# Performance work log

Measured on AMD Instinct MI355X. Metric: run time of the kernel, lower is better.

## Reference

```python
import jax, jax.numpy as jnp
import numpy as np
import math

DIM = 1024
SEQ = 4096
BATCH = 4
CHUNK = 64
LN_EPS = 1e-5


def setup_inputs() -> dict:
    key = jax.random.key(0)
    ks = jax.random.split(key, 16)
    d = DIM
    def lin(k):
        k1, k2 = jax.random.split(k)
        lim = 1.0 / math.sqrt(d)
        W = jax.random.uniform(k1, (d, d), jnp.float32, -lim, lim)
        b = jax.random.uniform(k2, (d,), jnp.float32, -lim, lim)
        return W, b
    Wk, bk = lin(ks[0])
    Wv, bv = lin(ks[1])
    Wq, bq = lin(ks[2])
    Wkm, bkm = lin(ks[3])
    Wqm, bqm = lin(ks[4])
    Wo, bo = lin(ks[5])
    return {
        "x": jax.random.normal(ks[6], (BATCH, SEQ, d), jnp.float32),
        "base_phases": jax.random.normal(ks[7], (SEQ, d), jnp.float32) * math.pi,
        "Wk": Wk, "bk": bk, "Wv": Wv, "bv": bv, "Wq": Wq, "bq": bq,
        "Wkm": Wkm, "bkm": bkm, "Wqm": Wqm, "bqm": bqm,
        "mod_scale": jnp.ones((1,), jnp.float32) * 0.1,
        "ln_g": jnp.ones((d,), jnp.float32),
        "ln_b": jnp.zeros((d,), jnp.float32),
        "Wo": Wo, "bo": bo,
    }


def reference(x, base_phases, Wk, bk, Wv, bv, Wq, bq, Wkm, bkm, Wqm, bqm,
              mod_scale, ln_g, ln_b, Wo, bo):
    B, S, D = x.shape
    key = x @ Wk + bk
    value = x @ Wv + bv
    query = x @ Wq + bq
    base = base_phases[:S][None]                      # [1,S,D]
    key_phase = base + (key @ Wkm + bkm) * mod_scale   # [B,S,D]
    query_phase = base + (query @ Wqm + bqm) * mod_scale
    bound_real = value * jnp.cos(key_phase)
    bound_imag = value * jnp.sin(key_phase)
    pad = (CHUNK - S % CHUNK) % CHUNK
    if pad > 0:
        pcfg = ((0, 0), (0, pad), (0, 0))
        bound_real = jnp.pad(bound_real, pcfg)
        bound_imag = jnp.pad(bound_imag, pcfg)
        query_phase = jnp.pad(query_phase, pcfg)
    P = S + pad
    nc = P // CHUNK
    br = bound_real.reshape(B, nc, CHUNK, D)
    bi = bound_imag.reshape(B, nc, CHUNK, D)
    qp = query_phase.reshape(B, nc, CHUNK, D)
    mem_real = jnp.cumsum(br, axis=2)
    mem_imag = jnp.cumsum(bi, axis=2)
    retrieved = mem_real * jnp.cos(qp) + mem_imag * jnp.sin(qp)
    retrieved = retrieved.reshape(B, P, D)[:, :S] / math.sqrt(D)
    mu = jnp.mean(retrieved, axis=-1, keepdims=True)
    var = jnp.mean(jnp.square(retrieved - mu), axis=-1, keepdims=True)
    normed = (retrieved - mu) * jax.lax.rsqrt(var + LN_EPS) * ln_g + ln_b
    out = normed @ Wo + bo
    return x + out
```

## Files before the change

### kernel.cpp

```cpp
#include <hip/hip_runtime.h>

#define DIM 1024
#define SEQ 4096
#define MROWS 16384
#define CHUNK 64
#define NCHUNKBLKS 256

typedef float  f32x4  __attribute__((ext_vector_type(4)));
typedef __bf16 bf16x8 __attribute__((ext_vector_type(8)));
typedef __bf16 bf16x4 __attribute__((ext_vector_type(4)));

__device__ __forceinline__ void gld16(const void* g, void* l) {
  __builtin_amdgcn_global_load_lds((__attribute__((address_space(1))) void*)g,
                                   (__attribute__((address_space(3))) void*)l,
                                   16, 0, 0);
}

__device__ __forceinline__ f32x4 ld4f(const __bf16* p) {
  bf16x4 v = *(const bf16x4*)p;
  f32x4 r;
#pragma unroll
  for (int j = 0; j < 4; ++j) r[j] = (float)v[j];
  return r;
}

template <int MODE, int NCOLT>
__global__ __launch_bounds__(512, 2)
void gemm256(const __bf16* __restrict__ A, const __bf16* __restrict__ Bt,
             const float* __restrict__ bias,
             __bf16* __restrict__ ob0, __bf16* __restrict__ ob1,
             __bf16* __restrict__ ob2,
             float* __restrict__ of, const float* __restrict__ xres)
{
  __shared__ __bf16 As[2][256 * 64];
  __shared__ __bf16 Bs[2][256 * 64];
  const int tid  = threadIdx.x;
  const int lane = tid & 63;
  const int widx = tid >> 6;
  const int wr = widx >> 2, wc = widx & 3;
  const int bx  = blockIdx.x;
  const int xcd = bx & 7, p = bx >> 3;
  const int row_t = (xcd << 3) + (p & 7);
  const int col_t = p >> 3;
  const int row0 = row_t * 256, col0 = col_t * 256;

  const int srow   = widx * 8 + (lane >> 3);
  const int schunk = (lane & 7) ^ ((lane >> 3) & 7);
  const __bf16* Ag = A  + (size_t)(row0 + srow) * DIM + schunk * 8;
  const __bf16* Bg = Bt + (size_t)(col0 + srow) * DIM + schunk * 8;

  f32x4 acc[8][4] = {};
  const int arb = wr * 128 + (lane & 15);
  const int brb = wc * 64  + (lane & 15);
  const int kg = lane >> 4;
  const int lx = lane & 7;

#define STG(kt_, bu_) { \
    const __bf16* a_ = Ag + (kt_) * 64; \
    const __bf16* b_ = Bg + (kt_) * 64; \
    char* ab_ = (char*)(&As[bu_][0]) + widx * 1024; \
    char* bb_ = (char*)(&Bs[bu_][0]) + widx * 1024; \
    _Pragma("unroll") for (int i_ = 0; i_ < 4; ++i_) { \
      gld16(a_ + i_ * 64 * DIM, ab_ + i_ * 8192); \
      gld16(b_ + i_ * 64 * DIM, bb_ + i_ * 8192); } }

  STG(0, 0)
  __syncthreads();
  for (int kt = 0; kt < 16; ++kt) {
    if (kt + 1 < 16) STG(kt + 1, (kt + 1) & 1)
    __builtin_amdgcn_sched_barrier(0);
    const bf16x8* Av = (const bf16x8*)(&As[kt & 1][0]);
    const bf16x8* Bv = (const bf16x8*)(&Bs[kt & 1][0]);
#pragma unroll
    for (int kk = 0; kk < 2; ++kk) {
      const int pc = (kk * 4 + kg) ^ lx;
      bf16x8 af[8], bf[4];
#pragma unroll
      for (int i = 0; i < 8; ++i) af[i] = Av[(arb + i * 16) * 8 + pc];
#pragma unroll
      for (int i = 0; i < 4; ++i) bf[i] = Bv[(brb + i * 16) * 8 + pc];
      __builtin_amdgcn_s_setprio(1);
#pragma unroll
      for (int mi = 0; mi < 8; ++mi)
#pragma unroll
        for (int ni = 0; ni < 4; ++ni)
          acc[mi][ni] = __builtin_amdgcn_mfma_f32_16x16x32_bf16(af[mi], bf[ni], acc[mi][ni], 0, 0, 0);
      __builtin_amdgcn_s_setprio(0);
    }
    __syncthreads();
  }
#undef STG

  const int ccol  = col0 + wc * 64 + (lane & 15);
  const int crow0 = row0 + wr * 128 + kg * 4;
  float bvv[4];
#pragma unroll
  for (int ni = 0; ni < 4; ++ni) bvv[ni] = bias[ccol + ni * 16];
  if (MODE == 0) {
    const int band = col_t >> 2;
    const int lcol0 = ccol & 1023;
    __bf16* outb = (band == 0) ? ob0 : (band == 1) ? ob1 : ob2;
#pragma unroll
    for (int mi = 0; mi < 8; ++mi)
#pragma unroll
      for (int ni = 0; ni < 4; ++ni)
#pragma unroll
        for (int r = 0; r < 4; ++r) {
          const int row = crow0 + mi * 16 + r;
          outb[(size_t)row * DIM + lcol0 + ni * 16] = (__bf16)(acc[mi][ni][r] + bvv[ni]);
        }
  } else {
#pragma unroll
    for (int mi = 0; mi < 8; ++mi)
#pragma unroll
      for (int ni = 0; ni < 4; ++ni)
#pragma unroll
        for (int r = 0; r < 4; ++r) {
          const int row = crow0 + mi * 16 + r;
          const size_t idx = (size_t)row * DIM + ccol + ni * 16;
          of[idx] = acc[mi][ni][r] + bvv[ni] + xres[idx];
        }
  }
}

#define KLOOP64(As_, Bs_, Ag_, Bg_, AsL_, BsL_)                                  \
  for (int kt = 0; kt < DIM / 64; ++kt) {                                        \
    const __bf16* a_ = Ag_ + kt * 64;                                            \
    const __bf16* b_ = Bg_ + kt * 64;                                            \
    _Pragma("unroll") for (int i = 0; i < 4; ++i) {                              \
      gld16(a_ + i * 32 * DIM, AsL_ + i * 4096);                                 \
      gld16(b_ + i * 32 * DIM, BsL_ + i * 4096);                                 \
    }                                                                            \
    __syncthreads();                                                             \
    const bf16x8* Av_ = (const bf16x8*)(As_);                                    \
    const bf16x8* Bv_ = (const bf16x8*)(Bs_);                                    \
    _Pragma("unroll") for (int kk = 0; kk < 2; ++kk) {                           \
      bf16x8 af[4], bfv[4];                                                      \
      const int pc = (kk * 4 + kg) ^ (lane & 7);                                 \
      _Pragma("unroll") for (int i = 0; i < 4; ++i) af[i]  = Av_[(ar + i*16)*8 + pc]; \
      _Pragma("unroll") for (int i = 0; i < 4; ++i) bfv[i] = Bv_[(br + i*16)*8 + pc]; \
      _Pragma("unroll") for (int mi = 0; mi < 4; ++mi)                           \
        _Pragma("unroll") for (int ni = 0; ni < 4; ++ni)                         \
          acc[mi][ni] = __builtin_amdgcn_mfma_f32_16x16x32_bf16(af[mi], bfv[ni], acc[mi][ni], 0, 0, 0); \
    }                                                                            \
    __syncthreads();                                                             \
  }

__global__ __launch_bounds__(256, 2)
void gemm_wc(const __bf16* __restrict__ A, const __bf16* __restrict__ Bt,
             void* __restrict__ outp, const float* __restrict__ mscp,
             const __bf16* __restrict__ A2, const __bf16* __restrict__ Bt2,
             void* __restrict__ out2)
{
  __shared__ __bf16 As[128 * 64];
  __shared__ __bf16 Bs[128 * 64];
  if (blockIdx.z == 1) { A = A2; Bt = Bt2; outp = out2; }
  const int row0 = blockIdx.y * 128, col0 = blockIdx.x * 128;
  const int tid  = threadIdx.x;
  const int lane = tid & 63;
  const int widx = tid >> 6;
  const int wr   = widx >> 1, wc = widx & 1;
  const int kc = ((lane & 7) ^ ((lane >> 3) & 7)) * 8;
  const __bf16* Ag = A  + (size_t)(row0 + widx * 8 + (lane >> 3)) * DIM + kc;
  const __bf16* Bg = Bt + (size_t)(col0 + widx * 8 + (lane >> 3)) * DIM + kc;
  char* AsL = (char*)As + widx * 1024;
  char* BsL = (char*)Bs + widx * 1024;
  f32x4 acc[4][4] = {};
  const int ar = wr * 64 + (lane & 15);
  const int br = wc * 64 + (lane & 15);
  const int kg = lane >> 4;

  KLOOP64(As, Bs, Ag, Bg, AsL, BsL)

  const int ccol = col0 + wc * 64 + (lane & 15);
  const int crow = row0 + wr * 64 + kg * 4;
  const float ms = mscp[0];
#pragma unroll
  for (int mi = 0; mi < 4; ++mi)
#pragma unroll
    for (int ni = 0; ni < 4; ++ni)
#pragma unroll
      for (int r = 0; r < 4; ++r) {
        const int row = crow + mi * 16 + r;
        const int col = ccol + ni * 16;
        ((__bf16*)outp)[(size_t)row * DIM + col] = (__bf16)(acc[mi][ni][r] * ms);
      }
}

__global__ __launch_bounds__(256)
void phasor_ln(const __bf16* __restrict__ val, const __bf16* __restrict__ kph,
               const __bf16* __restrict__ qph, const __bf16* __restrict__ baseb,
               const float* __restrict__ g, const float* __restrict__ lb,
               __bf16* __restrict__ nb)
{
  const int t = threadIdx.x;
  const int w = t >> 6, lane = t & 63;
  const size_t r0 = (size_t)blockIdx.x * CHUNK;
  const int c = t * 4;
  const f32x4 gv  = ((const f32x4*)g)[t];
  const f32x4 lbv = ((const f32x4*)lb)[t];
  __shared__ float redS[8][4], redQ[8][4];
  float mr[4] = {0.f, 0.f, 0.f, 0.f};
  float mi[4] = {0.f, 0.f, 0.f, 0.f};
  for (int rb = 0; rb < 8; ++rb) {
    float ret[8][4], ss[8], qq[8];
#pragma unroll
    for (int r = 0; r < 8; ++r) {
      const int row = rb * 8 + r;
      const size_t base = (r0 + row) * DIM + c;
      const f32x4 v  = ld4f(val + base);
      const f32x4 kp = ld4f(kph + base);
      const f32x4 qp = ld4f(qph + base);
      const f32x4 bp = ld4f(baseb + (size_t)((r0 + row) & (SEQ - 1)) * DIM + c);
      float s = 0.f, q = 0.f;
#pragma unroll
      for (int j = 0; j < 4; ++j) {
        float sk, ck, sq, cq;
        __sincosf(bp[j] + kp[j], &sk, &ck);
        mr[j] += v[j] * ck;
        mi[j] += v[j] * sk;
        __sincosf(bp[j] + qp[j], &sq, &cq);
        ret[r][j] = (mr[j] * cq + mi[j] * sq) * 0.03125f;
        s += ret[r][j];
        q += ret[r][j] * ret[r][j];
      }
      ss[r] = s; qq[r] = q;
    }
#pragma unroll
    for (int off = 32; off > 0; off >>= 1)
#pragma unroll
      for (int r = 0; r < 8; ++r) {
        ss[r] += __shfl_down(ss[r], off);
        qq[r] += __shfl_down(qq[r], off);
      }
    if (lane == 0)
#pragma unroll
      for (int r = 0; r < 8; ++r) { redS[r][w] = ss[r]; redQ[r][w] = qq[r]; }
    __syncthreads();
#pragma unroll
    for (int r = 0; r < 8; ++r) {
      const float mu   = (redS[r][0] + redS[r][1] + redS[r][2] + redS[r][3]) * (1.0f / DIM);
      const float varr = (redQ[r][0] + redQ[r][1] + redQ[r][2] + redQ[r][3]) * (1.0f / DIM) - mu * mu;
      const float rinv = rsqrtf(varr + 1e-5f);
      bf16x4 o;
#pragma unroll
      for (int j = 0; j < 4; ++j) o[j] = (__bf16)((ret[r][j] - mu) * rinv * gv[j] + lbv[j]);
      *(bf16x4*)(nb + (r0 + rb * 8 + r) * DIM + c) = o;
    }
    __syncthreads();
  }
}

__global__ void f2b_kernel(const float* __restrict__ in, __bf16* __restrict__ out, int n4) {
  int i = blockIdx.x * 256 + threadIdx.x;
  if (i >= n4) return;
  f32x4 vv = ((const f32x4*)in)[i];
  bf16x4 o;
#pragma unroll
  for (int j = 0; j < 4; ++j) o[j] = (__bf16)vv[j];
  ((bf16x4*)out)[i] = o;
}

__global__ void wrapb_kernel(const float* __restrict__ in, __bf16* __restrict__ out, int n4) {
  int i = blockIdx.x * 256 + threadIdx.x;
  if (i >= n4) return;
  f32x4 vv = ((const f32x4*)in)[i];
  bf16x4 o;
#pragma unroll
  for (int j = 0; j < 4; ++j) {
    float v = vv[j];
    v -= 6.2831853f * rintf(v * 0.15915494f);
    o[j] = (__bf16)v;
  }
  ((bf16x4*)out)[i] = o;
}

__global__ void f2b2_kernel(const float* __restrict__ i0, __bf16* __restrict__ o0,
                            const float* __restrict__ i1, __bf16* __restrict__ o1, int n4) {
  int i = blockIdx.x * 256 + threadIdx.x;
  if (i >= n4) return;
  const float* in = blockIdx.y ? i1 : i0;
  __bf16* out = blockIdx.y ? o1 : o0;
  f32x4 vv = ((const f32x4*)in)[i];
  bf16x4 o;
#pragma unroll
  for (int j = 0; j < 4; ++j) o[j] = (__bf16)vv[j];
  ((bf16x4*)out)[i] = o;
}

__global__ void transpose_f2b4(const float* __restrict__ s0, __bf16* __restrict__ d0,
                               const float* __restrict__ s1, __bf16* __restrict__ d1,
                               const float* __restrict__ s2, __bf16* __restrict__ d2,
                               const float* __restrict__ s3, __bf16* __restrict__ d3) {
  __shared__ float tle[32][33];
  const float* W; __bf16* Wt;
  switch (blockIdx.z) {
    case 0: W = s0; Wt = d0; break;
    case 1: W = s1; Wt = d1; break;
    case 2: W = s2; Wt = d2; break;
    default: W = s3; Wt = d3; break;
  }
  const int tx = threadIdx.x, ty = threadIdx.y;
  const int bx = blockIdx.x * 32, by = blockIdx.y * 32;
  for (int i = ty; i < 32; i += 8) tle[i][tx] = W[(size_t)(by + i) * DIM + bx + tx];
  __syncthreads();
  for (int i = ty; i < 32; i += 8) Wt[(size_t)(bx + i) * DIM + by + tx] = (__bf16)tle[tx][i];
}

__global__ void biasinit(const float* __restrict__ bv, const float* __restrict__ bkm,
                         const float* __restrict__ bqm, const float* __restrict__ ms,
                         float* __restrict__ biasAll) {
  const int n = blockIdx.x * 256 + threadIdx.x;
  const float m = ms[0];
  biasAll[n] = bv[n];
  biasAll[1024 + n] = bkm[n] * m;
  biasAll[2048 + n] = bqm[n] * m;
}

__global__ void biasacc(const float* __restrict__ bk, const float* __restrict__ Wkm,
                        const float* __restrict__ bq, const float* __restrict__ Wqm,
                        const float* __restrict__ ms, float* __restrict__ biasAll) {
  const int t = threadIdx.x;
  const int which = blockIdx.y;
  const int k0 = blockIdx.z * 128;
  const float* bs = which ? bq : bk;
  const float* W  = which ? Wqm : Wkm;
  const int n0 = t * 4;
  float s0 = 0.f, s1 = 0.f, s2 = 0.f, s3 = 0.f;
  for (int k = k0; k < k0 + 128; ++k) {
    const float b = bs[k];
    const f32x4 wv = *(const f32x4*)(W + (size_t)k * DIM + n0);
    s0 += b * wv[0]; s1 += b * wv[1]; s2 += b * wv[2]; s3 += b * wv[3];
  }
  const float m = ms[0];
  float* dst = biasAll + 1024 + which * 1024 + n0;
  atomicAdd(dst + 0, s0 * m);
  atomicAdd(dst + 1, s1 * m);
  atomicAdd(dst + 2, s2 * m);
  atomicAdd(dst + 3, s3 * m);
}

__global__ void copyx_kernel(const float* __restrict__ x, float* __restrict__ out, int n4) {
  int i = blockIdx.x * 256 + threadIdx.x;
  if (i >= n4) return;
  ((f32x4*)out)[i] = ((const f32x4*)x)[i];
}

extern "C" void kernel_launch(void* const* d_in, const int* in_sizes, int n_in,
                              void* d_out, int out_size, void* d_ws, size_t ws_size,
                              hipStream_t stream)
{
  (void)in_sizes; (void)n_in; (void)out_size;
  const float* x     = (const float*)d_in[0];
  const float* basep = (const float*)d_in[1];
  const float* Wk    = (const float*)d_in[2];
  const float* bk    = (const float*)d_in[3];
  const float* Wv    = (const float*)d_in[4];
  const float* bv    = (const float*)d_in[5];
  const float* Wq    = (const float*)d_in[6];
  const float* bq    = (const float*)d_in[7];
  const float* Wkm   = (const float*)d_in[8];
  const float* bkm   = (const float*)d_in[9];
  const float* Wqm   = (const float*)d_in[10];
  const float* bqm   = (const float*)d_in[11];
  const float* msc   = (const float*)d_in[12];
  const float* lng   = (const float*)d_in[13];
  const float* lnb   = (const float*)d_in[14];
  const float* Wo    = (const float*)d_in[15];
  const float* bo    = (const float*)d_in[16];

  char* ws = (char*)d_ws;
  const size_t MB = 1ull << 20;
  if (ws_size < 153 * MB) {
    copyx_kernel<<<MROWS * DIM / 4 / 256, 256, 0, stream>>>(x, (float*)d_out, MROWS * DIM / 4);
    return;
  }

  __bf16* xb     = (__bf16*)ws;
  __bf16* valb   = (__bf16*)(ws +  32 * MB);
  __bf16* kphb   = (__bf16*)(ws +  64 * MB);
  __bf16* qphb   = (__bf16*)(ws +  96 * MB);
  __bf16* Ball   = (__bf16*)(ws + 128 * MB);
  __bf16* WoT    = (__bf16*)(ws + 134 * MB);
  __bf16* TWkm   = (__bf16*)(ws + 136 * MB);
  __bf16* BWk    = (__bf16*)(ws + 138 * MB);
  __bf16* TWqm   = (__bf16*)(ws + 140 * MB);
  __bf16* BWq    = (__bf16*)(ws + 142 * MB);
  __bf16* baseb  = (__bf16*)(ws + 144 * MB);
  float*  biasAll= (float*)(ws + 152 * MB);
  __bf16* nbuf   = xb;

  f2b_kernel<<<MROWS * DIM / 4 / 256, 256, 0, stream>>>(x, xb, MROWS * DIM / 4);
  wrapb_kernel<<<SEQ * DIM / 4 / 256, 256, 0, stream>>>(basep, baseb, SEQ * DIM / 4);
  dim3 tg(32, 32, 4), tb(32, 8);
  transpose_f2b4<<<tg, tb, 0, stream>>>(Wv, Ball, Wo, WoT, Wkm, TWkm, Wqm, TWqm);
  f2b2_kernel<<<dim3(DIM * DIM / 4 / 256, 2), 256, 0, stream>>>(Wk, BWk, Wq, BWq, DIM * DIM / 4);
  gemm_wc<<<dim3(8, 8, 2), 256, 0, stream>>>(
      TWkm, BWk, Ball + (size_t)1024 * DIM, msc,
      TWqm, BWq, Ball + (size_t)2048 * DIM);
  biasinit<<<4, 256, 0, stream>>>(bv, bkm, bqm, msc, biasAll);
  biasacc<<<dim3(1, 2, 8), 256, 0, stream>>>(bk, Wkm, bq, Wqm, msc, biasAll);

  gemm256<0, 12><<<768, 512, 0, stream>>>(xb, Ball, biasAll,
                                          valb, kphb, qphb, nullptr, nullptr);
  phasor_ln<<<NCHUNKBLKS, 256, 0, stream>>>(valb, kphb, qphb, baseb, lng, lnb, nbuf);
  gemm256<1, 4><<<256, 512, 0, stream>>>(nbuf, WoT, bo,
                                         nullptr, nullptr, nullptr, (float*)d_out, x);
}
```

Measured before the change: 273.0 us.

## Prefetch two K-tiles ahead with explicit vmcnt waits in GEMM main loop

Restructures the double-buffered GEMM loop so two K-tiles are in flight. Each buffer is refilled right after it is consumed, and partial vmcnt waits replace the full __syncthreads drain. The goal is to hide global-to-LDS load latency behind the MFMA work rather than stalling every iteration on all outstanding loads. It adds a second barrier per tile and relies on hand-counted vmcnt values, which is fragile if the number of loads per stage changes.

Result: no change. 269.4 us (-1.3%).

```diff
diff --git a/kernel.cpp b/kernel.cpp
--- a/kernel.cpp
+++ b/kernel.cpp
@@ -64,31 +64,43 @@
       gld16(a_ + i_ * 64 * DIM, ab_ + i_ * 8192); \
       gld16(b_ + i_ * 64 * DIM, bb_ + i_ * 8192); } }
 
+#define GHALF(TI_, BU_, NG_) { \
+    const bf16x8* Av = (const bf16x8*)(&As[BU_][0]); \
+    const bf16x8* Bv = (const bf16x8*)(&Bs[BU_][0]); \
+    _Pragma("unroll") for (int kk = 0; kk < 2; ++kk) { \
+      const int pc = (kk * 4 + kg) ^ lx; \
+      bf16x8 af[8], bf[4]; \
+      _Pragma("unroll") for (int i = 0; i < 8; ++i) af[i] = Av[(arb + i * 16) * 8 + pc]; \
+      _Pragma("unroll") for (int i = 0; i < 4; ++i) bf[i] = Bv[(brb + i * 16) * 8 + pc]; \
+      __builtin_amdgcn_s_setprio(1); \
+      _Pragma("unroll") for (int mi = 0; mi < 8; ++mi) \
+        _Pragma("unroll") for (int ni = 0; ni < 4; ++ni) \
+          acc[mi][ni] = __builtin_amdgcn_mfma_f32_16x16x32_bf16(af[mi], bf[ni], acc[mi][ni], 0, 0, 0); \
+      __builtin_amdgcn_s_setprio(0); \
+    } \
+    asm volatile("s_waitcnt lgkmcnt(0)" ::: "memory"); \
+    __builtin_amdgcn_sched_barrier(0); \
+    __builtin_amdgcn_s_barrier();             \
+    if (NG_) { \
+      STG((TI_) + 2, BU_)                     \
+      asm volatile("s_waitcnt vmcnt(8)" ::: "memory");   \
+    } else { \
+      asm volatile("s_waitcnt vmcnt(0)" ::: "memory");   \
+    } \
+    __builtin_amdgcn_sched_barrier(0); \
+    __builtin_amdgcn_s_barrier();             \
+  }
+
   STG(0, 0)
-  __syncthreads();
-  for (int kt = 0; kt < 16; ++kt) {
-    if (kt + 1 < 16) STG(kt + 1, (kt + 1) & 1)
-    __builtin_amdgcn_sched_barrier(0);
-    const bf16x8* Av = (const bf16x8*)(&As[kt & 1][0]);
-    const bf16x8* Bv = (const bf16x8*)(&Bs[kt & 1][0]);
-#pragma unroll
-    for (int kk = 0; kk < 2; ++kk) {
-      const int pc = (kk * 4 + kg) ^ lx;
-      bf16x8 af[8], bf[4];
-#pragma unroll
-      for (int i = 0; i < 8; ++i) af[i] = Av[(arb + i * 16) * 8 + pc];
-#pragma unroll
-      for (int i = 0; i < 4; ++i) bf[i] = Bv[(brb + i * 16) * 8 + pc];
-      __builtin_amdgcn_s_setprio(1);
-#pragma unroll
-      for (int mi = 0; mi < 8; ++mi)
-#pragma unroll
-        for (int ni = 0; ni < 4; ++ni)
-          acc[mi][ni] = __builtin_amdgcn_mfma_f32_16x16x32_bf16(af[mi], bf[ni], acc[mi][ni], 0, 0, 0);
-      __builtin_amdgcn_s_setprio(0);
-    }
-    __syncthreads();
-  }
+  STG(1, 1)
+  asm volatile("s_waitcnt vmcnt(8)" ::: "memory");
+  __builtin_amdgcn_sched_barrier(0);
+  __builtin_amdgcn_s_barrier();
+  for (int ktp = 0; ktp < 8; ++ktp) {
+    GHALF(2 * ktp,     0, ktp < 7)
+    GHALF(2 * ktp + 1, 1, ktp < 7)
+  }
+#undef GHALF
 #undef STG
 
   const int ccol  = col0 + wc * 64 + (lane & 15);
```

## Interleave split global-to-LDS staging with quarter-tile MFMA phases in GEMM main loop

Applied to the files above, without the earlier changes.

Restructures the GEMM K-loop into four phases per tile. Each phase loads a subset of A/B fragments from LDS, issues one half-tile of the next tile's global-to-LDS copy, and runs a 16-MFMA block, with explicit barriers and vmcnt/lgkmcnt waits. The goal is to spread memory traffic across the compute and overlap loads with MFMA work, in the style of a ping-pong schedule, instead of issuing the whole next tile's loads up front. It adds many more barriers per tile and hand-tuned waitcnt placement, and the schedule could be fragile.

Measured after the change: 277.2 us. No clear change (+1.5%).

```diff
diff --git a/kernel.cpp b/kernel.cpp
--- a/kernel.cpp
+++ b/kernel.cpp
@@ -17,7 +17,7 @@
 }
 
 __device__ __forceinline__ f32x4 ld4f(const __bf16* p) {
-  bf16x4 v = *(const bf16x4*)p;
+  bf16x4 v = *(const bf16x4*)(p);
   f32x4 r;
 #pragma unroll
   for (int j = 0; j < 4; ++j) r[j] = (float)v[j];
@@ -48,6 +48,8 @@
   const int schunk = (lane & 7) ^ ((lane >> 3) & 7);
   const __bf16* Ag = A  + (size_t)(row0 + srow) * DIM + schunk * 8;
   const __bf16* Bg = Bt + (size_t)(col0 + srow) * DIM + schunk * 8;
+  char* AsB = (char*)As;
+  char* BsB = (char*)Bs;
 
   f32x4 acc[8][4] = {};
   const int arb = wr * 128 + (lane & 15);
@@ -55,41 +57,88 @@
   const int kg = lane >> 4;
   const int lx = lane & 7;
 
-#define STG(kt_, bu_) { \
-    const __bf16* a_ = Ag + (kt_) * 64; \
-    const __bf16* b_ = Bg + (kt_) * 64; \
-    char* ab_ = (char*)(&As[bu_][0]) + widx * 1024; \
-    char* bb_ = (char*)(&Bs[bu_][0]) + widx * 1024; \
-    _Pragma("unroll") for (int i_ = 0; i_ < 4; ++i_) { \
-      gld16(a_ + i_ * 64 * DIM, ab_ + i_ * 8192); \
-      gld16(b_ + i_ * 64 * DIM, bb_ + i_ * 8192); } }
-
-  STG(0, 0)
-  __syncthreads();
-  for (int kt = 0; kt < 16; ++kt) {
-    if (kt + 1 < 16) STG(kt + 1, (kt + 1) & 1)
-    __builtin_amdgcn_sched_barrier(0);
-    const bf16x8* Av = (const bf16x8*)(&As[kt & 1][0]);
-    const bf16x8* Bv = (const bf16x8*)(&Bs[kt & 1][0]);
-#pragma unroll
-    for (int kk = 0; kk < 2; ++kk) {
-      const int pc = (kk * 4 + kg) ^ lx;
-      bf16x8 af[8], bf[4];
-#pragma unroll
-      for (int i = 0; i < 8; ++i) af[i] = Av[(arb + i * 16) * 8 + pc];
-#pragma unroll
-      for (int i = 0; i < 4; ++i) bf[i] = Bv[(brb + i * 16) * 8 + pc];
-      __builtin_amdgcn_s_setprio(1);
-#pragma unroll
-      for (int mi = 0; mi < 8; ++mi)
-#pragma unroll
-        for (int ni = 0; ni < 4; ++ni)
-          acc[mi][ni] = __builtin_amdgcn_mfma_f32_16x16x32_bf16(af[mi], bf[ni], acc[mi][ni], 0, 0, 0);
-      __builtin_amdgcn_s_setprio(0);
-    }
-    __syncthreads();
-  }
-#undef STG
+#define STG_A(T_, H_) { \
+    const __bf16* g_ = Ag + (size_t)(H_) * 128 * DIM + (T_) * 64; \
+    char* d_ = AsB + (((T_) & 1) * 32768) + (H_) * 16384 + widx * 1024; \
+    gld16(g_, d_); gld16(g_ + 64 * DIM, d_ + 8192); }
+#define STG_B(T_, H_) { \
+    const __bf16* g_ = Bg + (size_t)(H_) * 128 * DIM + (T_) * 64; \
+    char* d_ = BsB + (((T_) & 1) * 32768) + (H_) * 16384 + widx * 1024; \
+    gld16(g_, d_); gld16(g_ + 64 * DIM, d_ + 8192); }
+
+#define SB  __builtin_amdgcn_sched_barrier(0);
+#define PSYNC_LG \
+    SB __builtin_amdgcn_s_barrier(); \
+    asm volatile("s_waitcnt lgkmcnt(0)" ::: "memory"); SB
+#define PEND \
+    SB __builtin_amdgcn_s_barrier(); SB
+
+#define Q16(AF_, BF_, MO_, NO_) \
+    __builtin_amdgcn_s_setprio(1); \
+    _Pragma("unroll") for (int kk = 0; kk < 2; ++kk) \
+      _Pragma("unroll") for (int mi = 0; mi < 4; ++mi) \
+        _Pragma("unroll") for (int ni = 0; ni < 2; ++ni) \
+          acc[(MO_) + mi][(NO_) + ni] = __builtin_amdgcn_mfma_f32_16x16x32_bf16( \
+              AF_[mi][kk], BF_[ni][kk], acc[(MO_) + mi][(NO_) + ni], 0, 0, 0); \
+    __builtin_amdgcn_s_setprio(0);
+
+#define DO_TILE(T_, G1_, G2_, VN_) { \
+    const bf16x8* Av = (const bf16x8*)(AsB + ((T_) & 1) * 32768); \
+    const bf16x8* Bv = (const bf16x8*)(BsB + ((T_) & 1) * 32768); \
+    bf16x8 a03[4][2], a47[4][2], b01[2][2], b23[2][2]; \
+     \
+    _Pragma("unroll") for (int kk = 0; kk < 2; ++kk) { \
+      const int pc = (kk * 4 + kg) ^ lx; \
+      _Pragma("unroll") for (int i = 0; i < 2; ++i) b01[i][kk] = Bv[(brb + i * 16) * 8 + pc]; \
+      _Pragma("unroll") for (int i = 0; i < 4; ++i) a03[i][kk] = Av[(arb + i * 16) * 8 + pc]; \
+    } \
+    if (G1_) STG_A((T_) + 1, 1) \
+    PSYNC_LG \
+    Q16(a03, b01, 0, 0) \
+    PEND \
+     \
+    _Pragma("unroll") for (int kk = 0; kk < 2; ++kk) { \
+      const int pc = (kk * 4 + kg) ^ lx; \
+      _Pragma("unroll") for (int i = 0; i < 2; ++i) b23[i][kk] = Bv[(brb + (2 + i) * 16) * 8 + pc]; \
+    } \
+    if (G1_) STG_B((T_) + 1, 0) \
+    PSYNC_LG \
+    Q16(a03, b23, 0, 2) \
+    PEND \
+     \
+    _Pragma("unroll") for (int kk = 0; kk < 2; ++kk) { \
+      const int pc = (kk * 4 + kg) ^ lx; \
+      _Pragma("unroll") for (int i = 0; i < 4; ++i) a47[i][kk] = Av[(arb + (4 + i) * 16) * 8 + pc]; \
+    } \
+    if (G1_) STG_B((T_) + 1, 1) \
+    PSYNC_LG \
+    Q16(a47, b01, 4, 0) \
+    PEND \
+     \
+    if (G2_) STG_A((T_) + 2, 0) \
+    SB __builtin_amdgcn_s_barrier(); SB \
+    Q16(a47, b23, 4, 2) \
+    SB \
+    if ((VN_) == 2)      { asm volatile("s_waitcnt vmcnt(2)" ::: "memory"); } \
+    else if ((VN_) == 0) { asm volatile("s_waitcnt vmcnt(0)" ::: "memory"); } \
+    SB __builtin_amdgcn_s_barrier(); SB \
+  }
+
+  STG_A(0, 0) STG_A(0, 1) STG_B(0, 0) STG_B(0, 1) STG_A(1, 0)
+  asm volatile("s_waitcnt vmcnt(2)" ::: "memory");
+  SB __builtin_amdgcn_s_barrier(); SB
+
+  for (int t = 0; t < 14; ++t) DO_TILE(t, 1, 1, 2)
+  DO_TILE(14, 1, 0, 0)
+  DO_TILE(15, 0, 0, -1)
+
+#undef DO_TILE
+#undef Q16
+#undef PEND
+#undef PSYNC_LG
+#undef SB
+#undef STG_A
+#undef STG_B
 
   const int ccol  = col0 + wc * 64 + (lane & 15);
   const int crow0 = row0 + wr * 128 + kg * 4;
```
